# Performance work log

Measured on AMD Instinct MI355X. Metric: run time of the kernel, lower is better.

The kernel has to match this reference:

```python
import jax, jax.numpy as jnp
import numpy as np

# Matryoshka config (torch module's bitwidth_options / bitwidth_weights)
BIT_OPTIONS = (8, 4, 2)
BIT_WEIGHTS = {8: 1.0, 4: 0.5, 2: 0.25}
MASTER = 8  # max(BIT_OPTIONS); matryoshka_slice hardcodes 8-bit master codes


def matryoshka_slice(q, slice_bw):
    # q: int candidate codes in [0, 2**MASTER - 1]
    drop = 8 - slice_bw
    floor = q >> drop
    maxv = (1 << slice_bw) - 1
    if MASTER == slice_bw:
        return jnp.clip(floor, 0, maxv)
    # torch: `x >> drop - 1 & 1` parses as `(x >> (drop - 1)) & 1`
    round_bit = (q >> (drop - 1)) & 1
    return jnp.clip(floor + round_bit, 0, maxv)


def dequantize(q, scale, zero, slice_bw):
    q_shifted = matryoshka_slice(q, slice_bw) << (MASTER - slice_bw)
    return scale * (q_shifted.astype(scale.dtype) - zero)


def setup_inputs() -> dict:
    key = jax.random.key(0)
    k1, k2 = jax.random.split(key)
    rows, cols = 1024, 256
    x = jax.random.normal(k1, (rows, cols), dtype=jnp.float32)
    # per-channel scale (nonzero, realistic small magnitudes) and symmetric zero-point
    scale = jax.random.uniform(k2, (rows, 1), dtype=jnp.float32, minval=0.01, maxval=0.05)
    zero = jnp.full((rows, 1), 128.0, dtype=jnp.float32)  # (maxq+1)/2 for sym quant
    return {"x": x, "scale": scale, "zero": zero, "maxq": 255}


def reference(x, scale, zero, maxq):
    # candidate codes: (maxq+1, 1, 1) broadcasting over x's (rows, cols)
    q = jnp.arange(maxq + 1, dtype=jnp.int32)[:, None, None]
    xb = x[None]  # (1, rows, cols)
    total_err = jnp.zeros((), dtype=x.dtype)
    loss = jnp.zeros((), dtype=x.dtype)
    for bw in BIT_OPTIONS:  # descending, matching the torch if-chain 8..2 accumulation order
        l = xb - dequantize(q, scale, zero, bw)  # (maxq+1, rows, cols)
        loss = loss + l
        total_err = total_err + BIT_WEIGHTS[bw] * (l * l)
    qweight = jnp.argmin(total_err, axis=0)  # (rows, cols) int
    loss_sel = jnp.take_along_axis(loss, qweight[None], axis=0)[0]
    return qweight.astype(jnp.uint8), loss_sel
```

## Files before the change

### kernel.cpp

```cpp
#include <hip/hip_runtime.h>


__device__ __forceinline__ constexpr int slice4(int q) {
    int v = (q >> 4) + ((q >> 3) & 1);
    return v > 15 ? 15 : v;
}
__device__ __forceinline__ constexpr int slice2(int q) {
    int v = (q >> 6) + ((q >> 5) & 1);
    return v > 3 ? 3 : v;
}

__global__ __launch_bounds__(256) void matryoshka_kernel(
    const float* __restrict__ x,
    const float* __restrict__ scale,
    const float* __restrict__ zero,
    float* __restrict__ out,
    int rows, int cols)
{
    const int row = blockIdx.x;
    const int col = threadIdx.x;
    const int idx = row * cols + col;

    const float s  = scale[row];
    const float z  = zero[row];
    const float nz = __fsub_rn(0.0f, z);
    const float xv = x[idx];

    float best = 3.402823466e38f;
    int bq = 0;

#pragma unroll
    for (int c = 0; c < 8; ++c) {
        const float K2 = (float)(slice2(c * 32) << 6);
        const float d2 = __fmul_rn(s, __fsub_rn(K2, z));
        const float l2 = __fsub_rn(xv, d2);
        const float h2 = __fmul_rn(0.25f, __fmul_rn(l2, l2));
#pragma unroll
        for (int b = 0; b < 4; ++b) {
            const int qa = c * 32 + b * 8;
            const float K4 = (float)(slice4(qa) << 4);
            const float d4 = __fmul_rn(s, __fsub_rn(K4, z));
            const float l4 = __fsub_rn(xv, d4);
            const float h4 = __fmul_rn(0.5f, __fmul_rn(l4, l4));
#pragma unroll
            for (int j = 0; j < 8; ++j) {
                const int q = qa + j;
                const float qmz = __fadd_rn((float)q, nz);
                const float l8  = __fsub_rn(xv, __fmul_rn(s, qmz));
                const float err = __fadd_rn(__fadd_rn(__fmul_rn(l8, l8), h4), h2);
                if (err < best) { best = err; bq = q; }
            }
        }
    }

    {
        const float qmz8 = __fadd_rn((float)bq, nz);
        const float l8 = __fsub_rn(xv, __fmul_rn(s, qmz8));

        int s4 = (bq >> 4) + ((bq >> 3) & 1); if (s4 > 15) s4 = 15;
        const float l4 = __fsub_rn(xv, __fmul_rn(s, __fsub_rn((float)(s4 << 4), z)));

        int s2 = (bq >> 6) + ((bq >> 5) & 1); if (s2 > 3) s2 = 3;
        const float l2 = __fsub_rn(xv, __fmul_rn(s, __fsub_rn((float)(s2 << 6), z)));

        const float loss = __fadd_rn(__fadd_rn(l8, l4), l2);

        out[idx] = (float)bq;
        out[rows * cols + idx] = loss;
    }
}

extern "C" void kernel_launch(void* const* d_in, const int* in_sizes, int n_in,
                              void* d_out, int out_size, void* d_ws, size_t ws_size,
                              hipStream_t stream) {
    const float* x     = (const float*)d_in[0];
    const float* scale = (const float*)d_in[1];
    const float* zero  = (const float*)d_in[2];

    float* out = (float*)d_out;

    const int rows = in_sizes[1];
    const int cols = in_sizes[0] / rows;

    matryoshka_kernel<<<rows, 256, 0, stream>>>(x, scale, zero, out, rows, cols);
}
```

Measured before the change: 69.94 us.

## Replace per-code inner search with clamped nearest 8-bit code per group

Instead of evaluating all 8 fine codes in each 8-code group, the kernel computes the nearest 8-bit code from x/s+z once and clamps it into each group's range, evaluating only one candidate per group (32 instead of 256). Error terms are rewritten with FMAs using a precomputed w = x + s*z. This cuts the compute-bound inner loop substantially, but the FMA contraction and the analytical rounding can change tie-breaking and argmin results compared with the exact per-code search.

```diff
diff --git a/kernel.cpp b/kernel.cpp
--- a/kernel.cpp
+++ b/kernel.cpp
@@ -1,4 +1,5 @@
 #include <hip/hip_runtime.h>
+#include <math.h>
 
 
 __device__ __forceinline__ constexpr int slice4(int q) {
@@ -23,8 +24,12 @@
 
     const float s  = scale[row];
     const float z  = zero[row];
-    const float nz = __fsub_rn(0.0f, z);
     const float xv = x[idx];
+
+    const float w  = __builtin_fmaf(s, z, xv);
+    const float ns = -s;
+
+    const int q8 = (int)rintf(__builtin_fmaf(xv, 1.0f / s, z));
 
     float best = 3.402823466e38f;
     int bq = 0;
@@ -32,30 +37,27 @@
 #pragma unroll
     for (int c = 0; c < 8; ++c) {
         const float K2 = (float)(slice2(c * 32) << 6);
-        const float d2 = __fmul_rn(s, __fsub_rn(K2, z));
-        const float l2 = __fsub_rn(xv, d2);
-        const float h2 = __fmul_rn(0.25f, __fmul_rn(l2, l2));
+        const float l2 = __builtin_fmaf(ns, K2, w);
+        const float h2 = 0.25f * (l2 * l2);
 #pragma unroll
         for (int b = 0; b < 4; ++b) {
             const int qa = c * 32 + b * 8;
             const float K4 = (float)(slice4(qa) << 4);
-            const float d4 = __fmul_rn(s, __fsub_rn(K4, z));
-            const float l4 = __fsub_rn(xv, d4);
-            const float h4 = __fmul_rn(0.5f, __fmul_rn(l4, l4));
-#pragma unroll
-            for (int j = 0; j < 8; ++j) {
-                const int q = qa + j;
-                const float qmz = __fadd_rn((float)q, nz);
-                const float l8  = __fsub_rn(xv, __fmul_rn(s, qmz));
-                const float err = __fadd_rn(__fadd_rn(__fmul_rn(l8, l8), h4), h2);
-                if (err < best) { best = err; bq = q; }
-            }
+            const float l4 = __builtin_fmaf(ns, K4, w);
+            const float h42 = __builtin_fmaf(0.5f * l4, l4, h2);
+
+            int qi = q8 < qa ? qa : q8;
+            qi = qi > qa + 7 ? qa + 7 : qi;
+
+            const float qf  = (float)qi;
+            const float l8  = __builtin_fmaf(ns, qf, w);
+            const float err = __builtin_fmaf(l8, l8, h42);
+            if (err < best) { best = err; bq = qi; }
         }
     }
 
     {
-        const float qmz8 = __fadd_rn((float)bq, nz);
-        const float l8 = __fsub_rn(xv, __fmul_rn(s, qmz8));
+        const float l8 = __fsub_rn(xv, __fmul_rn(s, __fsub_rn((float)bq, z)));
 
         int s4 = (bq >> 4) + ((bq >> 3) & 1); if (s4 > 15) s4 = 15;
         const float l4 = __fsub_rn(xv, __fmul_rn(s, __fsub_rn((float)(s4 << 4), z)));
```

Measured after the change: 61.80 us. -11.6%, faster.
